# Optimization experiments

Measured on AMD Instinct MI355X. Metric: run time of the kernel, lower is better.

The kernel has to match this reference:

```python
import jax, jax.numpy as jnp
import numpy as np

N_FEAT = 64      # number of continuous features
N_BINS = 255     # bin edges per feature (EBM default) -> 256 score slots incl. OOV
N_PAIRS = 32     # interaction terms
BATCH = 262144


def _bin_indices(edges, x):
    """TF Discretization (searchsorted right) + IntegerLookup(vocab=range(B), OOV->0).
    edges: [N, B] sorted per row; x: [batch, N] -> int32 [batch, N] in [0, B]."""
    idx = jax.vmap(lambda e, col: jnp.searchsorted(e, col, side='right'),
                   in_axes=(0, 1), out_axes=1)(edges, x)  # [batch, N], values 0..B
    B = edges.shape[1]
    # IntegerLookup: value v in {0..B-1} -> v+1 ; value B (not in vocab) -> OOV index 0
    return jnp.where(idx < B, idx + 1, 0)


def setup_inputs() -> dict:
    key = jax.random.key(0)
    ks = jax.random.split(key, 6)
    x = jax.random.normal(ks[0], (BATCH, N_FEAT), dtype=jnp.float32)
    edges = jnp.sort(jax.random.normal(ks[1], (N_FEAT, N_BINS), dtype=jnp.float32), axis=1)
    pair_edges = jnp.sort(jax.random.normal(ks[2], (N_FEAT, N_BINS), dtype=jnp.float32), axis=1)
    w = jax.random.normal(ks[3], (N_FEAT, N_BINS + 1), dtype=jnp.float32) * 0.1
    tables = jax.random.normal(ks[4], (N_PAIRS, N_BINS + 1, N_BINS + 1), dtype=jnp.float32) * 0.1
    pairs = jax.random.randint(ks[5], (N_PAIRS, 2), 0, N_FEAT, dtype=jnp.int32)
    bias = jnp.zeros((1,), dtype=jnp.float32)
    return {"x": x, "edges": edges, "w": w, "pair_edges": pair_edges,
            "pairs": pairs, "tables": tables, "bias": bias}


def reference(x, edges, w, pair_edges, pairs, tables, bias):
    # --- per-feature main effects: one_hot(idx) @ Dense(1) == gather w[f, idx] ---
    idx = _bin_indices(edges, x)                                  # [batch, N]
    feat = w[jnp.arange(N_FEAT)[None, :], idx]                    # [batch, N]
    # --- pairwise interactions: gather_nd on [L, R] lookup tables ---
    pidx = _bin_indices(pair_edges, x)                            # [batch, N]
    li = pidx[:, pairs[:, 0]]                                     # [batch, P]
    ri = pidx[:, pairs[:, 1]]                                     # [batch, P]
    inter = tables[jnp.arange(N_PAIRS)[None, :], li, ri]          # [batch, P]
    # --- BiasLayer: reduce_sum(concat, axis=1) + bias, then sigmoid ---
    logits = jnp.sum(feat, axis=1) + jnp.sum(inter, axis=1) + bias[0]
    return jax.nn.sigmoid(logits)                                  # [batch]
```

## Files before the change

kernel.cpp:

```cpp
#include <hip/hip_runtime.h>
#include <hip/hip_fp16.h>

#define NBINS 255
#define NPAIRS 32
#define BIGF 3.0e38f


__device__ __forceinline__ void prep_edge_elem(int i,
        const float* __restrict__ edges, const float* __restrict__ pair_edges,
        const float* __restrict__ w, float* __restrict__ ws) {
    int f = i >> 8, j = i & 255;
    float* E  = ws;
    float* PE = ws + 16384;
    float* ME = ws + 32768;
    float* MP = ws + 36864;
    float* CU = ws + 40960;
    float* CP = ws + 41984;
    __half* W = (__half*)(ws + 43008);
    E[i]  = (j < NBINS) ? edges[f * NBINS + j]      : BIGF;
    PE[i] = (j < NBINS) ? pair_edges[f * NBINS + j] : BIGF;
    int src = (j < 255) ? j + 1 : 0;
    W[i]  = __float2half(w[f * 256 + src]);
    if (j < 64) {
        int idx = 4 * j + 3;
        ME[f * 64 + j] = (idx < NBINS) ? edges[f * NBINS + idx]      : BIGF;
        MP[f * 64 + j] = (idx < NBINS) ? pair_edges[f * NBINS + idx] : BIGF;
    }
    if (j < 16) {
        CU[f * 16 + j] = (j < 15) ? edges[f * NBINS + 16 * j + 15]      : BIGF;
        CP[f * 16 + j] = (j < 15) ? pair_edges[f * NBINS + 16 * j + 15] : BIGF;
    }
}

__global__ void ebm_prep_all(const float* __restrict__ edges,
                             const float* __restrict__ pair_edges,
                             const float* __restrict__ w,
                             const float* __restrict__ tables,
                             float* __restrict__ ws,
                             unsigned short* __restrict__ T16o) {
    int i = blockIdx.x * blockDim.x + threadIdx.x;
    int b = i & 255, a = (i >> 8) & 255, p = i >> 16;
    int ra = (a < 255) ? a + 1 : 0;
    int rb = (b < 255) ? b + 1 : 0;
    T16o[i] = __half_as_ushort(__float2half(tables[(p << 16) + (ra << 8) + rb]));
    if (i < 16384) prep_edge_elem(i, edges, pair_edges, w, ws);
}

__global__ void ebm_prep(const float* __restrict__ edges,
                         const float* __restrict__ pair_edges,
                         const float* __restrict__ w,
                         float* __restrict__ ws) {
    int i = blockIdx.x * blockDim.x + threadIdx.x;
    prep_edge_elem(i, edges, pair_edges, w, ws);
}

__global__ void ebm_prep_tables(const float* __restrict__ tables,
                                unsigned short* __restrict__ o) {
    int i = blockIdx.x * blockDim.x + threadIdx.x;
    int b = i & 255, a = (i >> 8) & 255, p = i >> 16;
    int ra = (a < 255) ? a + 1 : 0;
    int rb = (b < 255) ? b + 1 : 0;
    o[i] = __half_as_ushort(__float2half(tables[(p << 16) + (ra << 8) + rb]));
}

__global__ __launch_bounds__(1024, 8) void ebm_unary(
    const float* __restrict__ x,
    float* __restrict__ ws) {

    __shared__ __align__(16) char smem[81920];
    float*  sE  = (float*)smem;
    float4* sME = (float4*)(smem + 65536);

    int tid = threadIdx.x;
    {
        const float4* w4 = (const float4*)ws;
        float4* dE = (float4*)sE;
#pragma unroll
        for (int k = 0; k < 4; ++k) dE[tid + 1024 * k] = w4[tid + 1024 * k];
        sME[tid] = w4[8192 + tid];
    }
    __syncthreads();

    const float*  CU = ws + 40960;
    const __half* Wg = (const __half*)(ws + 43008);
    int row = blockIdx.x * 1024 + tid;
    const float4* x4  = (const float4*)x + (size_t)row * 16;
    const float4* sE4 = (const float4*)sE;

    float acc = 0.f;
#pragma unroll
    for (int g = 0; g < 16; ++g) {
        float4 xg = x4[g];
        float xf[4] = {xg.x, xg.y, xg.z, xg.w};
        int t[4];
#pragma unroll
        for (int j = 0; j < 4; ++j) {
            const float* cu = CU + (4 * g + j) * 16;
            int tt = 0;
#pragma unroll
            for (int k = 0; k < 15; ++k) tt += (xf[j] >= cu[k]);
            t[j] = tt;
        }
        float4 mu[4];
#pragma unroll
        for (int j = 0; j < 4; ++j) mu[j] = sME[(4 * g + j) * 16 + t[j]];
        int lo[4];
        float4 fu[4];
#pragma unroll
        for (int j = 0; j < 4; ++j) {
            int m = (xf[j] >= mu[j].x) + (xf[j] >= mu[j].y) + (xf[j] >= mu[j].z);
            lo[j] = 4 * t[j] + m;
            fu[j] = sE4[(4 * g + j) * 64 + lo[j]];
        }
#pragma unroll
        for (int j = 0; j < 4; ++j) {
            int c = 4 * lo[j] + (xf[j] >= fu[j].x) + (xf[j] >= fu[j].y) +
                    (xf[j] >= fu[j].z) + (xf[j] >= fu[j].w);
            acc += __half2float(Wg[(4 * g + j) * 256 + c]);
        }
    }
    ws[51200 + row] = acc;
}

__global__ __launch_bounds__(1024, 8) void ebm_pairf(
    const float* __restrict__ x,
    const int*   __restrict__ pairs,
    const float* __restrict__ tables_f32,
    const float* __restrict__ bias,
    const float* __restrict__ ws,
    const __half* __restrict__ T16,
    int useT16,
    float* __restrict__ out) {

    __shared__ __align__(16) char smem[81920];
    float*  sPE = (float*)smem;
    float4* sMP = (float4*)(smem + 65536);

    int tid = threadIdx.x;
    {
        const float4* w4 = (const float4*)ws;
        float4* dP = (float4*)sPE;
#pragma unroll
        for (int k = 0; k < 4; ++k) dP[tid + 1024 * k] = w4[4096 + tid + 1024 * k];
        sMP[tid] = w4[9216 + tid];
    }
    unsigned long long mask = 0;
#pragma unroll 1
    for (int k = 0; k < 2 * NPAIRS; ++k) mask |= 1ull << pairs[k];
    __syncthreads();

    const float* CP = ws + 41984;
    int row = blockIdx.x * 1024 + tid;
    const float4* x4  = (const float4*)x + (size_t)row * 16;
    const float4* sP4 = (const float4*)sPE;

    unsigned pw[16];
#pragma unroll
    for (int g = 0; g < 16; ++g) {
        float4 xg = x4[g];
        float xf[4] = {xg.x, xg.y, xg.z, xg.w};
        unsigned pword = 0;
#pragma unroll
        for (int j = 0; j < 4; ++j) {
            int f = 4 * g + j;
            if ((mask >> f) & 1) {
                const float* cp = CP + f * 16;
                int tt = 0;
#pragma unroll
                for (int k = 0; k < 15; ++k) tt += (xf[j] >= cp[k]);
                float4 mp = sMP[f * 16 + tt];
                int m = (xf[j] >= mp.x) + (xf[j] >= mp.y) + (xf[j] >= mp.z);
                int l2 = 4 * tt + m;
                float4 fp = sP4[f * 64 + l2];
                int c2 = 4 * l2 + (xf[j] >= fp.x) + (xf[j] >= fp.y) +
                         (xf[j] >= fp.z) + (xf[j] >= fp.w);
                pword |= (unsigned)c2 << (8 * j);
            }
        }
        pw[g] = pword;
    }

    __syncthreads();
    unsigned* park = (unsigned*)smem;
#pragma unroll
    for (int k = 0; k < 16; ++k) park[tid * 17 + k] = pw[k];
    __syncthreads();

    const unsigned char* me = (const unsigned char*)smem + tid * 68;
    float acc = bias[0] + ws[51200 + row];
    if (useT16) {
#pragma unroll
        for (int p = 0; p < NPAIRS; ++p) {
            int a = pairs[2 * p], b = pairs[2 * p + 1];
            int li = me[a], ri = me[b];
            acc += __half2float(T16[(p << 16) + (li << 8) + ri]);
        }
    } else {
#pragma unroll
        for (int p = 0; p < NPAIRS; ++p) {
            int a = pairs[2 * p], b = pairs[2 * p + 1];
            int li = me[a], ri = me[b];
            int lb = (li < 255) ? li + 1 : 0, rb = (ri < 255) ? ri + 1 : 0;
            acc += tables_f32[(p << 16) + (lb << 8) + rb];
        }
    }
    out[row] = 1.0f / (1.0f + __expf(-acc));
}

__device__ __forceinline__ unsigned pick16(const unsigned* pw, int s) {
    unsigned v01 = (s & 1) ? pw[1]  : pw[0];
    unsigned v23 = (s & 1) ? pw[3]  : pw[2];
    unsigned v45 = (s & 1) ? pw[5]  : pw[4];
    unsigned v67 = (s & 1) ? pw[7]  : pw[6];
    unsigned v89 = (s & 1) ? pw[9]  : pw[8];
    unsigned vab = (s & 1) ? pw[11] : pw[10];
    unsigned vcd = (s & 1) ? pw[13] : pw[12];
    unsigned vef = (s & 1) ? pw[15] : pw[14];
    unsigned w0 = (s & 2) ? v23 : v01;
    unsigned w1 = (s & 2) ? v67 : v45;
    unsigned w2 = (s & 2) ? vab : v89;
    unsigned w3 = (s & 2) ? vef : vcd;
    unsigned u0 = (s & 4) ? w1 : w0;
    unsigned u1 = (s & 4) ? w3 : w2;
    return (s & 8) ? u1 : u0;
}

__global__ __launch_bounds__(1024) void ebm_mono(
    const float* __restrict__ x,
    const int*   __restrict__ pairs,
    const float* __restrict__ tables_f32,
    const float* __restrict__ bias,
    const float* __restrict__ ws,
    const __half* __restrict__ T16,
    int useT16,
    float*       __restrict__ out) {

    __shared__ float  sE[16384];
    __shared__ float  sPE[16384];
    __shared__ float4 sME[1024];
    __shared__ float4 sMP[1024];

    int tid = threadIdx.x;
    {
        const float4* w4 = (const float4*)ws;
        float4* dE = (float4*)sE;
        float4* dP = (float4*)sPE;
        for (int i = tid; i < 4096; i += 1024) {
            dE[i] = w4[i];
            dP[i] = w4[4096 + i];
        }
        sME[tid] = w4[8192 + tid];
        sMP[tid] = w4[9216 + tid];
    }
    const float*  CU = ws + 40960;
    const float*  CP = ws + 41984;
    const __half* Wg = (const __half*)(ws + 43008);
    float bias0 = bias[0];
    __syncthreads();

    int row = blockIdx.x * 1024 + tid;
    const float4* x4 = (const float4*)x + (size_t)row * 16;
    const float4* sE4 = (const float4*)sE;
    const float4* sP4 = (const float4*)sPE;

    float acc = 0.f;
    unsigned pw[16];
#pragma unroll
    for (int g = 0; g < 16; ++g) {
        float4 xg = x4[g];
        float xf[4] = {xg.x, xg.y, xg.z, xg.w};
        int t[4], t2[4];
#pragma unroll
        for (int j = 0; j < 4; ++j) {
            const float* cu = CU + (4 * g + j) * 16;
            int tt = 0;
#pragma unroll
            for (int k = 0; k < 15; ++k) tt += (xf[j] >= cu[k]);
            t[j] = tt;
        }
#pragma unroll
        for (int j = 0; j < 4; ++j) {
            const float* cp = CP + (4 * g + j) * 16;
            int tt = 0;
#pragma unroll
            for (int k = 0; k < 15; ++k) tt += (xf[j] >= cp[k]);
            t2[j] = tt;
        }
        float4 mu[4], mp[4];
#pragma unroll
        for (int j = 0; j < 4; ++j) mu[j] = sME[(4 * g + j) * 16 + t[j]];
#pragma unroll
        for (int j = 0; j < 4; ++j) mp[j] = sMP[(4 * g + j) * 16 + t2[j]];
        int lo[4], lo2[4];
        float4 fu[4], fp[4];
#pragma unroll
        for (int j = 0; j < 4; ++j) {
            int m = (xf[j] >= mu[j].x) + (xf[j] >= mu[j].y) + (xf[j] >= mu[j].z);
            lo[j] = 4 * t[j] + m;
            fu[j] = sE4[(4 * g + j) * 64 + lo[j]];
        }
#pragma unroll
        for (int j = 0; j < 4; ++j) {
            int m = (xf[j] >= mp[j].x) + (xf[j] >= mp[j].y) + (xf[j] >= mp[j].z);
            lo2[j] = 4 * t2[j] + m;
            fp[j] = sP4[(4 * g + j) * 64 + lo2[j]];
        }
#pragma unroll
        for (int j = 0; j < 4; ++j) {
            int c = 4 * lo[j] + (xf[j] >= fu[j].x) + (xf[j] >= fu[j].y) +
                    (xf[j] >= fu[j].z) + (xf[j] >= fu[j].w);
            acc += __half2float(Wg[(4 * g + j) * 256 + c]);
        }
        unsigned pword = 0;
#pragma unroll
        for (int j = 0; j < 4; ++j) {
            int c2 = 4 * lo2[j] + (xf[j] >= fp[j].x) + (xf[j] >= fp[j].y) +
                     (xf[j] >= fp[j].z) + (xf[j] >= fp[j].w);
            pword |= (unsigned)c2 << (8 * j);
        }
        pw[g] = pword;
    }

    if (useT16) {
#pragma unroll
        for (int p = 0; p < NPAIRS; ++p) {
            int a = pairs[2 * p], b = pairs[2 * p + 1];
            unsigned wa = pick16(pw, a >> 2);
            unsigned wb = pick16(pw, b >> 2);
            int li = (wa >> ((a & 3) * 8)) & 255;
            int ri = (wb >> ((b & 3) * 8)) & 255;
            acc += __half2float(T16[(p << 16) + (li << 8) + ri]);
        }
    } else {
#pragma unroll
        for (int p = 0; p < NPAIRS; ++p) {
            int a = pairs[2 * p], b = pairs[2 * p + 1];
            unsigned wa = pick16(pw, a >> 2);
            unsigned wb = pick16(pw, b >> 2);
            int li = (wa >> ((a & 3) * 8)) & 255;
            int ri = (wb >> ((b & 3) * 8)) & 255;
            int lb = (li < 255) ? li + 1 : 0;
            int rb = (ri < 255) ? ri + 1 : 0;
            acc += tables_f32[(p << 16) + (lb << 8) + rb];
        }
    }
    out[row] = 1.0f / (1.0f + __expf(-(acc + bias0)));
}

extern "C" void kernel_launch(void* const* d_in, const int* in_sizes, int n_in,
                              void* d_out, int out_size, void* d_ws, size_t ws_size,
                              hipStream_t stream) {
    const float* x          = (const float*)d_in[0];
    const float* edges      = (const float*)d_in[1];
    const float* w          = (const float*)d_in[2];
    const float* pair_edges = (const float*)d_in[3];
    const int*   pairs      = (const int*)d_in[4];
    const float* tables     = (const float*)d_in[5];
    const float* bias       = (const float*)d_in[6];
    float* out = (float*)d_out;
    float* ws  = (float*)d_ws;

    if (ws_size >= (size_t)5447680) {
        __half* T16 = (__half*)((char*)d_ws + 1253376);
        ebm_prep_all<<<2048, 1024, 0, stream>>>(edges, pair_edges, w, tables,
                                                ws, (unsigned short*)T16);
        ebm_unary<<<256, 1024, 0, stream>>>(x, ws);
        ebm_pairf<<<256, 1024, 0, stream>>>(x, pairs, tables, bias, ws, T16, 1, out);
    } else {
        int useT16 = (ws_size >= (size_t)4399104) ? 1 : 0;
        __half* T16 = (__half*)((char*)d_ws + 204800);
        ebm_prep<<<64, 256, 0, stream>>>(edges, pair_edges, w, ws);
        if (useT16) {
            ebm_prep_tables<<<2048, 1024, 0, stream>>>(tables, (unsigned short*)T16);
        }
        ebm_mono<<<256, 1024, 0, stream>>>(x, pairs, tables, bias, ws, T16, useT16, out);
    }
}
```

Measured before the change: 218.2 us.

## Run unary and pair branches concurrently in one kernel, add final sigmoid kernel

Merges the separate unary and pairwise kernels into one 512-block launch where interleaved block groups run either the unary branch or the pair branch for the same rows. The two branches can then overlap on the GPU instead of running back to back. Each branch writes a partial sum to workspace, and a small final kernel adds them with the bias and applies the sigmoid. The change also prefetches the next float4 of x inside the loop, and it needs more workspace, which raises the size threshold for the fast path.

Result: faster. 213.8 us (-2.0%).

```diff
diff --git a/kernel.cpp b/kernel.cpp
--- a/kernel.cpp
+++ b/kernel.cpp
@@ -63,148 +63,144 @@
     o[i] = __half_as_ushort(__float2half(tables[(p << 16) + (ra << 8) + rb]));
 }
 
-__global__ __launch_bounds__(1024, 8) void ebm_unary(
-    const float* __restrict__ x,
-    float* __restrict__ ws) {
-
-    __shared__ __align__(16) char smem[81920];
-    float*  sE  = (float*)smem;
-    float4* sME = (float4*)(smem + 65536);
-
-    int tid = threadIdx.x;
-    {
-        const float4* w4 = (const float4*)ws;
-        float4* dE = (float4*)sE;
-#pragma unroll
-        for (int k = 0; k < 4; ++k) dE[tid + 1024 * k] = w4[tid + 1024 * k];
-        sME[tid] = w4[8192 + tid];
-    }
-    __syncthreads();
-
-    const float*  CU = ws + 40960;
-    const __half* Wg = (const __half*)(ws + 43008);
-    int row = blockIdx.x * 1024 + tid;
-    const float4* x4  = (const float4*)x + (size_t)row * 16;
-    const float4* sE4 = (const float4*)sE;
-
-    float acc = 0.f;
-#pragma unroll
-    for (int g = 0; g < 16; ++g) {
-        float4 xg = x4[g];
-        float xf[4] = {xg.x, xg.y, xg.z, xg.w};
-        int t[4];
-#pragma unroll
-        for (int j = 0; j < 4; ++j) {
-            const float* cu = CU + (4 * g + j) * 16;
-            int tt = 0;
-#pragma unroll
-            for (int k = 0; k < 15; ++k) tt += (xf[j] >= cu[k]);
-            t[j] = tt;
-        }
-        float4 mu[4];
-#pragma unroll
-        for (int j = 0; j < 4; ++j) mu[j] = sME[(4 * g + j) * 16 + t[j]];
-        int lo[4];
-        float4 fu[4];
-#pragma unroll
-        for (int j = 0; j < 4; ++j) {
-            int m = (xf[j] >= mu[j].x) + (xf[j] >= mu[j].y) + (xf[j] >= mu[j].z);
-            lo[j] = 4 * t[j] + m;
-            fu[j] = sE4[(4 * g + j) * 64 + lo[j]];
-        }
-#pragma unroll
-        for (int j = 0; j < 4; ++j) {
-            int c = 4 * lo[j] + (xf[j] >= fu[j].x) + (xf[j] >= fu[j].y) +
-                    (xf[j] >= fu[j].z) + (xf[j] >= fu[j].w);
-            acc += __half2float(Wg[(4 * g + j) * 256 + c]);
-        }
-    }
-    ws[51200 + row] = acc;
-}
-
-__global__ __launch_bounds__(1024, 8) void ebm_pairf(
+__global__ __launch_bounds__(1024, 8) void ebm_work(
     const float* __restrict__ x,
     const int*   __restrict__ pairs,
-    const float* __restrict__ tables_f32,
-    const float* __restrict__ bias,
-    const float* __restrict__ ws,
     const __half* __restrict__ T16,
-    int useT16,
-    float* __restrict__ out) {
+    float* __restrict__ ws) {
 
     __shared__ __align__(16) char smem[81920];
-    float*  sPE = (float*)smem;
-    float4* sMP = (float4*)(smem + 65536);
 
     int tid = threadIdx.x;
-    {
-        const float4* w4 = (const float4*)ws;
-        float4* dP = (float4*)sPE;
-#pragma unroll
-        for (int k = 0; k < 4; ++k) dP[tid + 1024 * k] = w4[4096 + tid + 1024 * k];
-        sMP[tid] = w4[9216 + tid];
-    }
-    unsigned long long mask = 0;
+    int blk = blockIdx.x;
+    int branch = (blk >> 3) & 1;
+    int half   = ((blk >> 4) << 3) | (blk & 7);
+    int row    = half * 1024 + tid;
+    const float4* x4 = (const float4*)x + (size_t)row * 16;
+    const float4* w4 = (const float4*)ws;
+
+    if (branch == 0) {
+        float*  sE  = (float*)smem;
+        float4* sME = (float4*)(smem + 65536);
+        {
+            float4* dE = (float4*)sE;
+#pragma unroll
+            for (int k = 0; k < 4; ++k) dE[tid + 1024 * k] = w4[tid + 1024 * k];
+            sME[tid] = w4[8192 + tid];
+        }
+        __syncthreads();
+
+        const float*  CUc = ws + 40960;
+        const __half* Wg  = (const __half*)(ws + 43008);
+        const float4* sE4 = (const float4*)sE;
+
+        float acc = 0.f;
+        float4 xg = x4[0];
+#pragma unroll
+        for (int g = 0; g < 16; ++g) {
+            float4 xnext = xg;
+            if (g < 15) xnext = x4[g + 1];
+            float xf[4] = {xg.x, xg.y, xg.z, xg.w};
+            int t[4];
+#pragma unroll
+            for (int j = 0; j < 4; ++j) {
+                const float* cu = CUc + (4 * g + j) * 16;
+                int tt = 0;
+#pragma unroll
+                for (int k = 0; k < 15; ++k) tt += (xf[j] >= cu[k]);
+                t[j] = tt;
+            }
+            float4 mu[4];
+#pragma unroll
+            for (int j = 0; j < 4; ++j) mu[j] = sME[(4 * g + j) * 16 + t[j]];
+            int lo[4];
+            float4 fu[4];
+#pragma unroll
+            for (int j = 0; j < 4; ++j) {
+                int m = (xf[j] >= mu[j].x) + (xf[j] >= mu[j].y) + (xf[j] >= mu[j].z);
+                lo[j] = 4 * t[j] + m;
+                fu[j] = sE4[(4 * g + j) * 64 + lo[j]];
+            }
+#pragma unroll
+            for (int j = 0; j < 4; ++j) {
+                int c = 4 * lo[j] + (xf[j] >= fu[j].x) + (xf[j] >= fu[j].y) +
+                        (xf[j] >= fu[j].z) + (xf[j] >= fu[j].w);
+                acc += __half2float(Wg[(4 * g + j) * 256 + c]);
+            }
+            xg = xnext;
+        }
+        ws[51200 + row] = acc;
+    } else {
+        float*  sPE = (float*)smem;
+        float4* sMP = (float4*)(smem + 65536);
+        {
+            float4* dP = (float4*)sPE;
+#pragma unroll
+            for (int k = 0; k < 4; ++k) dP[tid + 1024 * k] = w4[4096 + tid + 1024 * k];
+            sMP[tid] = w4[9216 + tid];
+        }
+        unsigned long long mask = 0;
 #pragma unroll 1
-    for (int k = 0; k < 2 * NPAIRS; ++k) mask |= 1ull << pairs[k];
-    __syncthreads();
-
-    const float* CP = ws + 41984;
-    int row = blockIdx.x * 1024 + tid;
-    const float4* x4  = (const float4*)x + (size_t)row * 16;
-    const float4* sP4 = (const float4*)sPE;
-
-    unsigned pw[16];
-#pragma unroll
-    for (int g = 0; g < 16; ++g) {
-        float4 xg = x4[g];
-        float xf[4] = {xg.x, xg.y, xg.z, xg.w};
-        unsigned pword = 0;
-#pragma unroll
-        for (int j = 0; j < 4; ++j) {
-            int f = 4 * g + j;
-            if ((mask >> f) & 1) {
-                const float* cp = CP + f * 16;
-                int tt = 0;
-#pragma unroll
-                for (int k = 0; k < 15; ++k) tt += (xf[j] >= cp[k]);
-                float4 mp = sMP[f * 16 + tt];
-                int m = (xf[j] >= mp.x) + (xf[j] >= mp.y) + (xf[j] >= mp.z);
-                int l2 = 4 * tt + m;
-                float4 fp = sP4[f * 64 + l2];
-                int c2 = 4 * l2 + (xf[j] >= fp.x) + (xf[j] >= fp.y) +
-                         (xf[j] >= fp.z) + (xf[j] >= fp.w);
-                pword |= (unsigned)c2 << (8 * j);
+        for (int k = 0; k < 2 * NPAIRS; ++k) mask |= 1ull << pairs[k];
+        __syncthreads();
+
+        const float* CPc = ws + 41984;
+        const float4* sP4 = (const float4*)sPE;
+
+        unsigned pw[16];
+        float4 xg = x4[0];
+#pragma unroll
+        for (int g = 0; g < 16; ++g) {
+            float4 xnext = xg;
+            if (g < 15) xnext = x4[g + 1];
+            float xf[4] = {xg.x, xg.y, xg.z, xg.w};
+            unsigned pword = 0;
+#pragma unroll
+            for (int j = 0; j < 4; ++j) {
+                int f = 4 * g + j;
+                if ((mask >> f) & 1) {
+                    const float* cp = CPc + f * 16;
+                    int tt = 0;
+#pragma unroll
+                    for (int k = 0; k < 15; ++k) tt += (xf[j] >= cp[k]);
+                    float4 mp = sMP[f * 16 + tt];
+                    int m = (xf[j] >= mp.x) + (xf[j] >= mp.y) + (xf[j] >= mp.z);
+                    int l2 = 4 * tt + m;
+                    float4 fp = sP4[f * 64 + l2];
+                    int c2 = 4 * l2 + (xf[j] >= fp.x) + (xf[j] >= fp.y) +
+                             (xf[j] >= fp.z) + (xf[j] >= fp.w);
+                    pword |= (unsigned)c2 << (8 * j);
+                }
             }
-        }
-        pw[g] = pword;
-    }
-
-    __syncthreads();
-    unsigned* park = (unsigned*)smem;
-#pragma unroll
-    for (int k = 0; k < 16; ++k) park[tid * 17 + k] = pw[k];
-    __syncthreads();
-
-    const unsigned char* me = (const unsigned char*)smem + tid * 68;
-    float acc = bias[0] + ws[51200 + row];
-    if (useT16) {
+            pw[g] = pword;
+            xg = xnext;
+        }
+
+        __syncthreads();
+        unsigned* park = (unsigned*)smem;
+#pragma unroll
+        for (int k = 0; k < 16; ++k) park[tid * 17 + k] = pw[k];
+        __syncthreads();
+
+        const unsigned char* me = (const unsigned char*)smem + tid * 68;
+        float acc = 0.f;
 #pragma unroll
         for (int p = 0; p < NPAIRS; ++p) {
             int a = pairs[2 * p], b = pairs[2 * p + 1];
             int li = me[a], ri = me[b];
             acc += __half2float(T16[(p << 16) + (li << 8) + ri]);
         }
-    } else {
-#pragma unroll
-        for (int p = 0; p < NPAIRS; ++p) {
-            int a = pairs[2 * p], b = pairs[2 * p + 1];
-            int li = me[a], ri = me[b];
-            int lb = (li < 255) ? li + 1 : 0, rb = (ri < 255) ? ri + 1 : 0;
-            acc += tables_f32[(p << 16) + (lb << 8) + rb];
-        }
-    }
-    out[row] = 1.0f / (1.0f + __expf(-acc));
+        ws[313344 + row] = acc;
+    }
+}
+
+__global__ __launch_bounds__(1024) void ebm_final(
+    const float* __restrict__ ws,
+    const float* __restrict__ bias,
+    float* __restrict__ out) {
+    int i = blockIdx.x * 1024 + threadIdx.x;
+    float z = ws[51200 + i] + ws[313344 + i] + bias[0];
+    out[i] = 1.0f / (1.0f + __expf(-z));
 }
 
 __device__ __forceinline__ unsigned pick16(const unsigned* pw, int s) {
@@ -360,12 +356,12 @@
     float* out = (float*)d_out;
     float* ws  = (float*)d_ws;
 
-    if (ws_size >= (size_t)5447680) {
-        __half* T16 = (__half*)((char*)d_ws + 1253376);
+    if (ws_size >= (size_t)6496256) {
+        __half* T16 = (__half*)((char*)d_ws + 2301952);
         ebm_prep_all<<<2048, 1024, 0, stream>>>(edges, pair_edges, w, tables,
                                                 ws, (unsigned short*)T16);
-        ebm_unary<<<256, 1024, 0, stream>>>(x, ws);
-        ebm_pairf<<<256, 1024, 0, stream>>>(x, pairs, tables, bias, ws, T16, 1, out);
+        ebm_work<<<512, 1024, 0, stream>>>(x, pairs, T16, ws);
+        ebm_final<<<256, 1024, 0, stream>>>(ws, bias, out);
     } else {
         int useT16 = (ws_size >= (size_t)4399104) ? 1 : 0;
         __half* T16 = (__half*)((char*)d_ws + 204800);
```
